# Performance work log

Hardware: AMD Instinct MI355X
Metric: run time of the kernel (lower is better)

Reference implementation:

```python
import jax, jax.numpy as jnp
import numpy as np

B, E, H, OUT, T = 256, 256, 256, 702, 512


def setup_inputs() -> dict:
    key = jax.random.key(0)
    ks = jax.random.split(key, 7)
    s = 1.0 / np.sqrt(H)  # PyTorch LSTM init scale
    return {
        "embed": jax.random.normal(ks[0], (B, 1, E), jnp.float32),
        "W_ih": jax.random.normal(ks[1], (4 * H, E), jnp.float32) * s,
        "W_hh": jax.random.normal(ks[2], (4 * H, H), jnp.float32) * s,
        "b_ih": jax.random.normal(ks[3], (4 * H,), jnp.float32) * s,
        "b_hh": jax.random.normal(ks[4], (4 * H,), jnp.float32) * s,
        "W_rec": jax.random.normal(ks[5], (OUT, H), jnp.float32) * s,
        "b_rec": jax.random.normal(ks[6], (OUT,), jnp.float32) * s,
        "sequence_length": T,
    }


def reference(embed, W_ih, W_hh, b_ih, b_hh, W_rec, b_rec, sequence_length):
    # embed: [B, 1, E]; decoder_type == 3 -> next input = out + embed
    x0 = embed[:, 0, :]  # [B, E]
    batch = x0.shape[0]
    hdim = W_hh.shape[1]

    def step(carry, _):
        h, c, x = carry
        gates = x @ W_ih.T + b_ih + h @ W_hh.T + b_hh  # [B, 4H]
        i, f, g, o = jnp.split(gates, 4, axis=-1)  # PyTorch gate order i,f,g,o
        c = jax.nn.sigmoid(f) * c + jax.nn.sigmoid(i) * jnp.tanh(g)
        h = jax.nn.sigmoid(o) * jnp.tanh(c)
        x_next = h + x0  # decoder_type 3 feedback
        return (h, c, x_next), h

    h0 = jnp.zeros((batch, hdim), embed.dtype)
    c0 = jnp.zeros((batch, hdim), embed.dtype)
    _, hs = jax.lax.scan(step, (h0, c0, x0), None, length=sequence_length)
    sequence_decoded = jnp.transpose(hs, (1, 0, 2))  # [B, T, H]
    sequence_reconstructed = sequence_decoded @ W_rec.T + b_rec  # [B, T, 702]
    return sequence_reconstructed, sequence_decoded
```

## Files before the change

### kernel.cpp

```cpp
#include <hip/hip_runtime.h>
#include <hip/hip_bf16.h>

#define B_   256
#define E_   256
#define H_   256
#define T_   512
#define OUT_ 702
#define G4H  1024

typedef _Float16 half8 __attribute__((ext_vector_type(8)));
typedef float    floatx4 __attribute__((ext_vector_type(4)));
typedef unsigned long long ull;

#define OFF_DTF    0
#define OFF_HBUF   4096
#define OFF_BASE   (4096 + 524288)
#define OFF_WC16   (OFF_BASE + 1048576)
#define OFF_WREC16 (OFF_WC16 + 524288)
#define OFF_HS16   (OFF_WREC16 + 360448)

__device__ __forceinline__ float ldin(const void* p, long i, int bf) {
  return bf ? __bfloat162float(((const __hip_bfloat16*)p)[i]) : ((const float*)p)[i];
}
__device__ __forceinline__ void stout(void* p, long i, float v, int bf) {
  if (bf) ((__hip_bfloat16*)p)[i] = __float2bfloat16(v);
  else    ((float*)p)[i] = v;
}
__device__ __forceinline__ float sigf(float x)  { return 1.0f / (1.0f + __expf(-x)); }
__device__ __forceinline__ float tanh_(float x) { float e = __expf(2.0f * x); return 1.0f - 2.0f / (e + 1.0f); }

__global__ void k_detect(const unsigned int* emb, int* dtf) {
  int tid = threadIdx.x;
  int cnt = 0;
  for (int i = tid; i < 256; i += 64) {
    unsigned int u = emb[i];
    unsigned int e = (u >> 7) & 0xFF;
    cnt += (e >= 100 && e <= 129) ? 1 : 0;
  }
  for (int off = 32; off > 0; off >>= 1) cnt += __shfl_down(cnt, off);
  if (tid == 0) *dtf = (cnt >= 128) ? 1 : 0;
}

__global__ void k_prep_wc(const void* wih, const void* whh, _Float16* wc, const int* dtf) {
  int bf = *dtf;
  long i = (long)blockIdx.x * 256 + threadIdx.x;
  wc[i] = (_Float16)(ldin(wih, i, bf) + ldin(whh, i, bf));
}

__global__ void k_prep_wrec(const void* wrec, _Float16* wr, const int* dtf) {
  int bf = *dtf;
  long i = (long)blockIdx.x * 256 + threadIdx.x;
  wr[i] = (i < (long)OUT_ * H_) ? (_Float16)ldin(wrec, i, bf) : (_Float16)0.0f;
}

__global__ void k_prep_base(const void* emb, const void* wih, const void* bih,
                            const void* bhh, float* base, const int* dtf) {
  int bf = *dtf;
  int b = blockIdx.x >> 2;
  int n = (blockIdx.x & 3) * 256 + threadIdx.x;
  __shared__ float x0s[256];
  x0s[threadIdx.x] = ldin(emb, (long)b * E_ + threadIdx.x, bf);
  __syncthreads();
  float acc = ldin(bih, n, bf) + ldin(bhh, n, bf);
  const long wrow = (long)n * E_;
  for (int k = 0; k < E_; ++k) acc += x0s[k] * ldin(wih, wrow + k, bf);
  base[(long)b * G4H + n] = acc;
}

__global__ void __launch_bounds__(256) k_lstm(char* ws, void* dout, const int* dtf) {
  const int bf  = *dtf;
  const int tid = threadIdx.x;
  const int g   = blockIdx.x >> 4;
  const int mem = blockIdx.x & 15;
  const int wid = tid >> 6;
  const int lane = tid & 63;
  const int q = lane >> 4;
  const int r = lane & 15;

  _Float16* wc   = (_Float16*)(ws + OFF_WC16);
  float*    base = (float*)(ws + OFF_BASE);
  ull*      hbuf = (ull*)(ws + OFF_HBUF);
  _Float16* hs16 = (_Float16*)(ws + OFF_HS16);

  half8 wfrag[8];
  {
    const long wrow = (long)(wid * 256 + mem * 16 + r) * H_;
#pragma unroll
    for (int kb = 0; kb < 8; ++kb)
      wfrag[kb] = *(const half8*)(wc + wrow + kb * 32 + q * 8);
  }

  const int m  = tid >> 4;
  const int jl = tid & 15;
  float basev[4];
  {
    const long brow = (long)(g * 16 + m) * G4H + mem * 16 + jl;
#pragma unroll
    for (int ty = 0; ty < 4; ++ty) basev[ty] = base[brow + ty * 256];
  }

  __shared__ _Float16 h_lds[16][264];
  __shared__ float gates_lds[16][68];
  for (int i = tid; i < 16 * 264; i += 256) (&h_lds[0][0])[i] = (_Float16)0.0f;
  float c = 0.0f;
  __syncthreads();

  const long out2off = (long)B_ * T_ * OUT_;
  const long orow_base = ((long)(g * 16 + m) * T_) * H_ + mem * 16 + jl;

  const bool packer = ((jl & 3) == 0);
  const int pword = (g * 16 + m) * 64 + mem * 4 + (jl >> 2);
  const int grow = g * 16 + wid * 4;

  for (int t = 0; t < T_; ++t) {
    floatx4 acc = {0.f, 0.f, 0.f, 0.f};
#pragma unroll
    for (int kb = 0; kb < 8; ++kb) {
      half8 a = *(const half8*)(&h_lds[r][kb * 32 + q * 8]);
      acc = __builtin_amdgcn_mfma_f32_16x16x32_f16(a, wfrag[kb], acc, 0, 0, 0);
    }
#pragma unroll
    for (int e = 0; e < 4; ++e) gates_lds[q * 4 + e][wid * 16 + r] = acc[e];
    __syncthreads();

    float gi = gates_lds[m][jl]      + basev[0];
    float gf = gates_lds[m][16 + jl] + basev[1];
    float gg = gates_lds[m][32 + jl] + basev[2];
    float go = gates_lds[m][48 + jl] + basev[3];
    c = sigf(gf) * c + sigf(gi) * tanh_(gg);
    float h = sigf(go) * tanh_(c);

    if (t < T_ - 1) {
      const int slot = t & 3;
      union { _Float16 f; unsigned short u; } cv; cv.f = (_Float16)h;
      unsigned int hu = cv.u;
      const int lb = lane & ~3;
      unsigned int u0 = __shfl(hu, lb);
      unsigned int u1 = __shfl(hu, lb + 1);
      unsigned int u2 = __shfl(hu, lb + 2);
      unsigned int u3 = __shfl(hu, lb + 3);
      if (packer) {
        if (t >= 2)
          __hip_atomic_store(&hbuf[((long)((t - 2) & 3) << 14) + pword], 0ULL,
                             __ATOMIC_RELAXED, __HIP_MEMORY_SCOPE_AGENT);
        ull w = (ull)(u0 & 0xFFFFu)
              | ((ull)(u1 & 0xFFFFu) << 16)
              | ((ull)(u2 & 0xFFFFu) << 32)
              | ((ull)(u3 & 0xFFFFu) << 48);
        __hip_atomic_store(&hbuf[((long)slot << 14) + pword], ~w,
                           __ATOMIC_RELAXED, __HIP_MEMORY_SCOPE_AGENT);
      }

      stout(dout, out2off + orow_base + (long)t * H_, h, bf);
      hs16[orow_base + (long)t * H_] = (_Float16)h;

      const ull* sb = hbuf + ((long)slot << 14);
      ull d[4] = {0, 0, 0, 0};
      unsigned int pend = 0xFu;
      int guard = 0;
      while (pend) {
        const unsigned int snap = pend;
        ull tmp[4];
#pragma unroll
        for (int i = 0; i < 4; ++i)
          if (snap & (1u << i))
            tmp[i] = __hip_atomic_load(&sb[(long)(grow + i) * 64 + lane],
                                       __ATOMIC_RELAXED, __HIP_MEMORY_SCOPE_AGENT);
#pragma unroll
        for (int i = 0; i < 4; ++i)
          if (snap & (1u << i)) {
            if (tmp[i]) { d[i] = ~tmp[i]; pend &= ~(1u << i); }
          }
        ++guard;
        if (guard > 256) __builtin_amdgcn_s_sleep(1);
        if (guard > 500000) break;
      }
      asm volatile("s_waitcnt vmcnt(0)" ::: "memory");
#pragma unroll
      for (int i = 0; i < 4; ++i)
        *(ull*)(&h_lds[wid * 4 + i][lane * 4]) = d[i];
      __syncthreads();
    } else {
      stout(dout, out2off + orow_base + (long)t * H_, h, bf);
      hs16[orow_base + (long)t * H_] = (_Float16)h;
    }
  }
}

__global__ void __launch_bounds__(256) k_proj(const char* ws, const void* brec,
                                              void* dout, const int* dtf) {
  const int bf  = *dtf;
  const int tid = threadIdx.x;
  const int wid = tid >> 6, lane = tid & 63, q = lane >> 4, r = lane & 15;
  const int mb = blockIdx.x & 2047, nb = blockIdx.x >> 11;
  const long mbase = (long)mb * 64;
  const int  nbase = nb * 192;
  const _Float16* hs16 = (const _Float16*)(ws + OFF_HS16);
  const _Float16* wr16 = (const _Float16*)(ws + OFF_WREC16);

  __shared__ _Float16 a_lds[64][264];
#pragma unroll
  for (int i = 0; i < 8; ++i) {
    int u = tid + i * 256;
    int row = u >> 5, c8 = (u & 31) * 8;
    half8 v = *(const half8*)(hs16 + (mbase + row) * H_ + c8);
    *(half8*)(&a_lds[row][c8]) = v;
  }
  __syncthreads();

  half8 bfrag[3][8];
  float bias[3];
#pragma unroll
  for (int j = 0; j < 3; ++j) {
    int ncol = nbase + (wid * 3 + j) * 16 + r;
    bias[j] = 0.0f;
    if (ncol < 704) {
      const long wrow = (long)ncol * H_;
#pragma unroll
      for (int kb = 0; kb < 8; ++kb)
        bfrag[j][kb] = *(const half8*)(wr16 + wrow + kb * 32 + q * 8);
    } else {
      half8 z = {0, 0, 0, 0, 0, 0, 0, 0};
#pragma unroll
      for (int kb = 0; kb < 8; ++kb) bfrag[j][kb] = z;
    }
    if (ncol < OUT_) bias[j] = ldin(brec, ncol, bf);
  }

  floatx4 acc[3][4];
#pragma unroll
  for (int j = 0; j < 3; ++j)
#pragma unroll
    for (int ms = 0; ms < 4; ++ms) acc[j][ms] = (floatx4){0.f, 0.f, 0.f, 0.f};

#pragma unroll
  for (int ms = 0; ms < 4; ++ms) {
#pragma unroll
    for (int kb = 0; kb < 8; ++kb) {
      half8 a = *(const half8*)(&a_lds[ms * 16 + r][kb * 32 + q * 8]);
#pragma unroll
      for (int j = 0; j < 3; ++j)
        acc[j][ms] = __builtin_amdgcn_mfma_f32_16x16x32_f16(a, bfrag[j][kb], acc[j][ms], 0, 0, 0);
    }
  }

#pragma unroll
  for (int j = 0; j < 3; ++j) {
    int ncol = nbase + (wid * 3 + j) * 16 + r;
    if (ncol >= OUT_) continue;
#pragma unroll
    for (int ms = 0; ms < 4; ++ms) {
#pragma unroll
      for (int e = 0; e < 4; ++e) {
        long mrow = mbase + ms * 16 + q * 4 + e;
        stout(dout, mrow * (long)OUT_ + ncol, acc[j][ms][e] + bias[j], bf);
      }
    }
  }
}

extern "C" void kernel_launch(void* const* d_in, const int* in_sizes, int n_in,
                              void* d_out, int out_size, void* d_ws, size_t ws_size,
                              hipStream_t stream) {
  const void* embed = d_in[0];
  const void* W_ih  = d_in[1];
  const void* W_hh  = d_in[2];
  const void* b_ih  = d_in[3];
  const void* b_hh  = d_in[4];
  const void* W_rec = d_in[5];
  const void* b_rec = d_in[6];
  char* ws = (char*)d_ws;
  const int* dtf = (const int*)(ws + OFF_DTF);

  hipMemsetAsync(ws, 0, OFF_BASE, stream);
  k_detect<<<1, 64, 0, stream>>>((const unsigned int*)embed, (int*)(ws + OFF_DTF));
  k_prep_wc<<<1024, 256, 0, stream>>>(W_ih, W_hh, (_Float16*)(ws + OFF_WC16), dtf);
  k_prep_wrec<<<704, 256, 0, stream>>>(W_rec, (_Float16*)(ws + OFF_WREC16), dtf);
  k_prep_base<<<1024, 256, 0, stream>>>(embed, W_ih, b_ih, b_hh, (float*)(ws + OFF_BASE), dtf);
  k_lstm<<<256, 256, 0, stream>>>(ws, d_out, dtf);
  k_proj<<<8192, 256, 0, stream>>>(ws, b_rec, d_out, dtf);
}
```

Measured before the change: 1.682 ms.

## Exchange LSTM gates via lane shuffles and double-buffer h in LDS

Remaps the W_hh fragment columns so that each wave's MFMA output tile holds all four gates (i,f,g,o) for the same hidden columns. The four gates for a column are then gathered with cross-lane shuffles instead of a round trip through a gates LDS array plus a block-wide barrier. The h LDS buffer is double-buffered so the per-step barrier count drops to one. The spin-wait now starts sleeping after fewer polls, which lowers polling pressure but may add wake-up latency on the critical path.

Measured after the change: 1.711 ms. No clear change (+1.7%).

```diff
diff --git a/kernel.cpp b/kernel.cpp
--- a/kernel.cpp
+++ b/kernel.cpp
@@ -76,59 +76,72 @@
   const int lane = tid & 63;
   const int q = lane >> 4;
   const int r = lane & 15;
+  const int gid = r >> 2;
+  const int cl  = r & 3;
 
   _Float16* wc   = (_Float16*)(ws + OFF_WC16);
   float*    base = (float*)(ws + OFF_BASE);
   ull*      hbuf = (ull*)(ws + OFF_HBUF);
   _Float16* hs16 = (_Float16*)(ws + OFF_HS16);
 
+  const int mycol = mem * 16 + wid * 4 + cl;
+  const int myrow = q * 4 + gid;
+
   half8 wfrag[8];
   {
-    const long wrow = (long)(wid * 256 + mem * 16 + r) * H_;
+    const long wrow = (long)(gid * 256 + mycol) * H_;
 #pragma unroll
     for (int kb = 0; kb < 8; ++kb)
       wfrag[kb] = *(const half8*)(wc + wrow + kb * 32 + q * 8);
   }
-
-  const int m  = tid >> 4;
-  const int jl = tid & 15;
   float basev[4];
   {
-    const long brow = (long)(g * 16 + m) * G4H + mem * 16 + jl;
-#pragma unroll
-    for (int ty = 0; ty < 4; ++ty) basev[ty] = base[brow + ty * 256];
-  }
-
-  __shared__ _Float16 h_lds[16][264];
-  __shared__ float gates_lds[16][68];
-  for (int i = tid; i < 16 * 264; i += 256) (&h_lds[0][0])[i] = (_Float16)0.0f;
+    const long brow = (long)(g * 16 + myrow) * G4H + mycol;
+#pragma unroll
+    for (int G = 0; G < 4; ++G) basev[G] = base[brow + G * 256];
+  }
+
+  __shared__ _Float16 h_lds[2][16][264];
+  for (int i = tid; i < 2 * 16 * 264; i += 256) (&h_lds[0][0][0])[i] = (_Float16)0.0f;
   float c = 0.0f;
   __syncthreads();
 
   const long out2off = (long)B_ * T_ * OUT_;
-  const long orow_base = ((long)(g * 16 + m) * T_) * H_ + mem * 16 + jl;
-
-  const bool packer = ((jl & 3) == 0);
-  const int pword = (g * 16 + m) * 64 + mem * 4 + (jl >> 2);
+  const long orow_base = ((long)(g * 16 + myrow) * T_) * H_ + mycol;
+
+  const bool packer = (cl == 0);
+  const int pword = (g * 16 + myrow) * 64 + mem * 4 + wid;
   const int grow = g * 16 + wid * 4;
 
+  int cur = 0;
   for (int t = 0; t < T_; ++t) {
     floatx4 acc = {0.f, 0.f, 0.f, 0.f};
 #pragma unroll
     for (int kb = 0; kb < 8; ++kb) {
-      half8 a = *(const half8*)(&h_lds[r][kb * 32 + q * 8]);
+      half8 a = *(const half8*)(&h_lds[cur][r][kb * 32 + q * 8]);
       acc = __builtin_amdgcn_mfma_f32_16x16x32_f16(a, wfrag[kb], acc, 0, 0, 0);
     }
-#pragma unroll
-    for (int e = 0; e < 4; ++e) gates_lds[q * 4 + e][wid * 16 + r] = acc[e];
-    __syncthreads();
-
-    float gi = gates_lds[m][jl]      + basev[0];
-    float gf = gates_lds[m][16 + jl] + basev[1];
-    float gg = gates_lds[m][32 + jl] + basev[2];
-    float go = gates_lds[m][48 + jl] + basev[3];
-    c = sigf(gf) * c + sigf(gi) * tanh_(gg);
-    float h = sigf(go) * tanh_(c);
+    float a0 = acc[0], a1 = acc[1], a2 = acc[2], a3 = acc[3];
+    float own = gid == 0 ? a0 : gid == 1 ? a1 : gid == 2 ? a2 : a3;
+    float vi = own, vf = own, vg = own, vo = own;
+#pragma unroll
+    for (int cc = 1; cc < 4; ++cc) {
+      int sg = (gid + cc) & 3;
+      float sv = sg == 0 ? a0 : sg == 1 ? a1 : sg == 2 ? a2 : a3;
+      int src = (lane & 48) + (((gid - cc) & 3) << 2) + cl;
+      float rv = __shfl(sv, src);
+      int rg = (gid - cc) & 3;
+      vi = (rg == 0) ? rv : vi;
+      vf = (rg == 1) ? rv : vf;
+      vg = (rg == 2) ? rv : vg;
+      vo = (rg == 3) ? rv : vo;
+    }
+    float giv = vi + basev[0];
+    float gfv = vf + basev[1];
+    float ggv = vg + basev[2];
+    float gov = vo + basev[3];
+    c = sigf(gfv) * c + sigf(giv) * tanh_(ggv);
+    float h = sigf(gov) * tanh_(c);
 
     if (t < T_ - 1) {
       const int slot = t & 3;
@@ -172,14 +185,16 @@
             if (tmp[i]) { d[i] = ~tmp[i]; pend &= ~(1u << i); }
           }
         ++guard;
-        if (guard > 256) __builtin_amdgcn_s_sleep(1);
+        if (guard > 64) __builtin_amdgcn_s_sleep(1);
         if (guard > 500000) break;
       }
       asm volatile("s_waitcnt vmcnt(0)" ::: "memory");
+      const int nxt = cur ^ 1;
 #pragma unroll
       for (int i = 0; i < 4; ++i)
-        *(ull*)(&h_lds[wid * 4 + i][lane * 4]) = d[i];
+        *(ull*)(&h_lds[nxt][wid * 4 + i][lane * 4]) = d[i];
       __syncthreads();
+      cur = nxt;
     } else {
       stout(dout, out2off + orow_base + (long)t * H_, h, bf);
       hs16[orow_base + (long)t * H_] = (_Float16)h;
```
